# Optimization experiments

Measured on AMD Instinct MI355X. Metric: run time of the kernel, lower is better.

The kernel has to match this reference:

```python
import jax, jax.numpy as jnp
import numpy as np

EMB = 1024
HID = 4096
B = 2
T = 4096
NUM_BLOCK = 24
EPS = 1e-6


def rmsnorm(x):
    # unparameterized RMS normalization over last dim
    return x * jax.lax.rsqrt(jnp.mean(jnp.square(x), axis=-1, keepdims=True) + EPS)


def setup_inputs() -> dict:
    key = jax.random.key(0)
    k1, k2, k3, k4 = jax.random.split(key, 4)
    x = jax.random.normal(k1, (B, T, EMB), dtype=jnp.float32)
    W1 = 0.02 * jax.random.normal(k2, (HID, EMB), dtype=jnp.float32)
    W2 = 0.02 * jax.random.normal(k3, (HID, EMB), dtype=jnp.float32)
    W3 = (0.02 / np.sqrt(NUM_BLOCK)) * jax.random.normal(k4, (EMB, HID), dtype=jnp.float32)
    return {"x": x, "W1": W1, "W2": W2, "W3": W3}


def bar_quadratic_causal_preact_stable(a, b):
    # y_t = (1/t^2) * sum_{i<=t} sum_{j<=t} exp(a_i + b_j), per feature channel.
    # exp factorizes, so compute stably via log-cumsum-exp along the seq axis.
    seq = a.shape[1]
    log_t = jnp.log(jnp.arange(1, seq + 1, dtype=a.dtype))  # [T]
    la = jax.lax.cumlogsumexp(a, axis=1)  # [B,T,H]
    lb = jax.lax.cumlogsumexp(b, axis=1)  # [B,T,H]
    return jnp.exp(la + lb - 2.0 * log_t[None, :, None])


def reference(x, W1, W2, W3):
    r = rmsnorm(x)
    a = jnp.einsum('bte,he->bth', r, W1)  # fc_1, no bias
    b = jnp.einsum('bte,he->bth', r, W2)  # fc_2, no bias
    r = bar_quadratic_causal_preact_stable(a, b)
    r = rmsnorm(r)
    r = jnp.einsum('bth,eh->bte', r, W3)  # fc_3, no bias
    return x + r
```

## Files before the change

kernel.cpp:

```cpp
#include <hip/hip_runtime.h>
#include <hip/hip_fp8.h>

#define EMB 1024
#define HID 4096
#define NB 2
#define TT 4096
#define MROWS (NB*TT)
#define N1 (2*HID)
#define CHUNK 128
#define NCH 32

typedef short short8 __attribute__((ext_vector_type(8)));
typedef float v4f   __attribute__((ext_vector_type(4)));
typedef int   v4i   __attribute__((ext_vector_type(4)));
typedef int   v8i   __attribute__((ext_vector_type(8)));

__device__ __forceinline__ unsigned short f2bf(float f) {
  unsigned int u = __float_as_uint(f);
  u += 0x7FFFu + ((u >> 16) & 1u);
  return (unsigned short)(u >> 16);
}
__device__ __forceinline__ float bf2f(unsigned short s) {
  return __uint_as_float(((unsigned int)s) << 16);
}
__device__ __forceinline__ unsigned char f2e4m3(float f) {
  __hip_fp8_e4m3 q(f);
  return *(unsigned char*)&q;
}
__device__ __forceinline__ float e4m32f(unsigned char c) {
  __hip_fp8_e4m3 q = *(__hip_fp8_e4m3*)&c;
  return (float)q;
}
__device__ __forceinline__ void g2l16(const void* g, void* l) {
  __builtin_amdgcn_global_load_lds(
      (const __attribute__((address_space(1))) void*)g,
      (__attribute__((address_space(3))) void*)l, 16, 0, 0);
}

__device__ __forceinline__ float block_reduce_sum(float v, float* sbuf) {
  #pragma unroll
  for (int off = 32; off; off >>= 1) v += __shfl_down(v, off, 64);
  int lane = threadIdx.x & 63, w = threadIdx.x >> 6;
  if (lane == 0) sbuf[w] = v;
  __syncthreads();
  return sbuf[0] + sbuf[1] + sbuf[2] + sbuf[3];
}

__global__ __launch_bounds__(256) void conv_all(const float* __restrict__ W1,
                                                const float* __restrict__ W2,
                                                const float* __restrict__ W3,
                                                unsigned short* __restrict__ o12,
                                                unsigned char* __restrict__ o3) {
  size_t i = ((size_t)blockIdx.x*256 + threadIdx.x)*4;
  if (i < 2ull*HID*EMB) {
    const float* s = (i < (size_t)HID*EMB) ? (W1 + i) : (W2 + (i - (size_t)HID*EMB));
    float4 v = *(const float4*)s;
    ushort4 u; u.x=f2bf(v.x); u.y=f2bf(v.y); u.z=f2bf(v.z); u.w=f2bf(v.w);
    *(ushort4*)(o12 + i) = u;
  } else {
    size_t off = i - 2ull*HID*EMB;
    float4 v = *(const float4*)(W3 + off);
    uchar4 u; u.x=f2e4m3(v.x*64.f); u.y=f2e4m3(v.y*64.f);
             u.z=f2e4m3(v.z*64.f); u.w=f2e4m3(v.w*64.f);
    *(uchar4*)(o3 + off) = u;
  }
}

__global__ __launch_bounds__(256) void rmsnorm_x(const float* __restrict__ x,
                                                 unsigned short* __restrict__ r) {
  __shared__ float sbuf[4];
  int row = blockIdx.x;
  float4 v = *(const float4*)(x + (size_t)row*EMB + threadIdx.x*4);
  float ss = v.x*v.x + v.y*v.y + v.z*v.z + v.w*v.w;
  float tot = block_reduce_sum(ss, sbuf);
  float sc = rsqrtf(tot * (1.0f/EMB) + 1e-6f);
  ushort4 o; o.x=f2bf(v.x*sc); o.y=f2bf(v.y*sc); o.z=f2bf(v.z*sc); o.w=f2bf(v.w*sc);
  *(ushort4*)(r + (size_t)row*EMB + threadIdx.x*4) = o;
}

__global__ __launch_bounds__(256) void normq(const unsigned short* __restrict__ y,
                                             unsigned char* __restrict__ y8) {
  __shared__ float sbuf[4];
  int row = blockIdx.x;
  const unsigned short* p = y + (size_t)row*HID + threadIdx.x*16;
  short8 v0 = *(const short8*)p;
  short8 v1 = *(const short8*)(p+8);
  float f[16]; float ss = 0.f;
  #pragma unroll
  for (int j=0;j<8;++j){ f[j]=bf2f((unsigned short)v0[j]); f[j+8]=bf2f((unsigned short)v1[j]); }
  #pragma unroll
  for (int j=0;j<16;++j) ss += f[j]*f[j];
  float tot = block_reduce_sum(ss, sbuf);
  float sc = rsqrtf(tot*(1.0f/HID) + 1e-6f);
  unsigned int w[4];
  #pragma unroll
  for (int g=0; g<4; ++g) {
    unsigned int a0 = f2e4m3(f[g*4+0]*sc);
    unsigned int a1 = f2e4m3(f[g*4+1]*sc);
    unsigned int a2 = f2e4m3(f[g*4+2]*sc);
    unsigned int a3 = f2e4m3(f[g*4+3]*sc);
    w[g] = a0 | (a1<<8) | (a2<<16) | (a3<<24);
  }
  uint4 o; o.x=w[0]; o.y=w[1]; o.z=w[2]; o.w=w[3];
  *(uint4*)(y8 + (size_t)row*HID + threadIdx.x*16) = o;
}

__global__ __launch_bounds__(256, 2)
void gemm_exp(const unsigned short* __restrict__ A,
              const unsigned short* __restrict__ Bt,
              unsigned char* __restrict__ C8,
              float* __restrict__ part,
              int K, int N) {
  __shared__ short lA[128*64];
  __shared__ short lB[128*64];
  const int tid  = threadIdx.x;
  const int lane = tid & 63;
  const int wm   = (tid >> 6) >> 1, wn = (tid >> 6) & 1;
  const int bid  = blockIdx.x;
  const int s0i  = bid >> 3;
  const int rowTile = s0i >> 3;
  const int colTile = ((bid & 7) << 3) | (s0i & 7);
  const int rowBase = rowTile * 128;
  const int colBase = colTile * 128;

  v4f acc[4][4];
  #pragma unroll
  for (int i=0;i<4;++i)
    #pragma unroll
    for (int j=0;j<4;++j) acc[i][j] = (v4f){0.f,0.f,0.f,0.f};

  for (int k0 = 0; k0 < K; k0 += 64) {
    #pragma unroll
    for (int j = 0; j < 4; ++j) {
      int s = j*256 + tid;
      int m = s >> 3;
      int c = (s & 7) ^ (m & 7);
      g2l16(A + (size_t)(rowBase + m)*K + k0 + c*8, &lA[s*8]);
    }
    #pragma unroll
    for (int j = 0; j < 4; ++j) {
      int s = j*256 + tid;
      int m = s >> 3;
      int c = (s & 7) ^ (m & 7);
      g2l16(Bt + (size_t)(colBase + m)*K + k0 + c*8, &lB[s*8]);
    }
    __syncthreads();
    #pragma unroll
    for (int s2 = 0; s2 < 2; ++s2) {
      const int quad = lane >> 4;
      const int cc = s2*4 + quad;
      short8 aF[4], bF[4];
      #pragma unroll
      for (int mt = 0; mt < 4; ++mt) {
        int ml = wm*64 + mt*16 + (lane & 15);
        aF[mt] = *(const short8*)&lA[(ml*8 + (cc ^ (ml & 7)))*8];
      }
      #pragma unroll
      for (int nt = 0; nt < 4; ++nt) {
        int nl = wn*64 + nt*16 + (lane & 15);
        bF[nt] = *(const short8*)&lB[(nl*8 + (cc ^ (nl & 7)))*8];
      }
      #pragma unroll
      for (int mt = 0; mt < 4; ++mt)
        #pragma unroll
        for (int nt = 0; nt < 4; ++nt)
          acc[mt][nt] = __builtin_amdgcn_mfma_f32_16x16x32_bf16(aF[mt], bF[nt], acc[mt][nt], 0, 0, 0);
    }
    __syncthreads();
  }

  const int quad = lane >> 4, c15 = lane & 15;
  float csum[4] = {0.f, 0.f, 0.f, 0.f};
  #pragma unroll
  for (int mt = 0; mt < 4; ++mt) {
    #pragma unroll
    for (int nt = 0; nt < 4; ++nt) {
      int col = colBase + wn*64 + nt*16 + c15;
      #pragma unroll
      for (int r = 0; r < 4; ++r) {
        int row = rowBase + wm*64 + mt*16 + quad*4 + r;
        size_t idx = (size_t)row*N + col;
        float e = __expf(acc[mt][nt][r]);
        C8[idx] = f2e4m3(e);
        csum[nt] += e;
      }
    }
  }
  float* cs = (float*)lA;
  #pragma unroll
  for (int nt = 0; nt < 4; ++nt) {
    float s = csum[nt];
    s += __shfl_xor(s, 16, 64);
    s += __shfl_xor(s, 32, 64);
    if (lane < 16) cs[wm*128 + wn*64 + nt*16 + lane] = s;
  }
  __syncthreads();
  if (tid < 128)
    part[(size_t)(colBase + tid)*64 + rowTile] = cs[tid] + cs[128 + tid];
}

__global__ __launch_bounds__(256, 2)
void gemm_out(const unsigned char* __restrict__ A8,
              const unsigned char* __restrict__ B8,
              const float* __restrict__ x,
              float* __restrict__ out,
              int K, int N) {
  __shared__ unsigned char lA8[128*128];
  __shared__ unsigned char lB8[128*128];
  const int tid  = threadIdx.x;
  const int lane = tid & 63;
  const int wm   = (tid >> 6) >> 1, wn = (tid >> 6) & 1;
  const int rowBase = blockIdx.x * 128;
  const int colBase = blockIdx.y * 128;
  const int q   = lane >> 4;
  const int r15 = lane & 15;

  v4f acc[4][4];
  #pragma unroll
  for (int i=0;i<4;++i)
    #pragma unroll
    for (int j=0;j<4;++j) acc[i][j] = (v4f){0.f,0.f,0.f,0.f};

  for (int k0 = 0; k0 < K; k0 += 128) {
    #pragma unroll
    for (int j = 0; j < 4; ++j) {
      int s = j*256 + tid;
      int m = s >> 3;
      int c = (s & 7) ^ (m & 7);
      g2l16(A8 + (size_t)(rowBase + m)*K + k0 + c*16, &lA8[s*16]);
    }
    #pragma unroll
    for (int j = 0; j < 4; ++j) {
      int s = j*256 + tid;
      int m = s >> 3;
      int c = (s & 7) ^ (m & 7);
      g2l16(B8 + (size_t)(colBase + m)*K + k0 + c*16, &lB8[s*16]);
    }
    __syncthreads();
    v8i aF[4], bF[4];
    #pragma unroll
    for (int mt = 0; mt < 4; ++mt) {
      int ml = wm*64 + mt*16 + r15;
      int s  = ml & 7;
      v4i lo = *(const v4i*)&lA8[ml*128 + (((2*q)   ^ s)<<4)];
      v4i hi = *(const v4i*)&lA8[ml*128 + (((2*q+1) ^ s)<<4)];
      aF[mt] = __builtin_shufflevector(lo, hi, 0,1,2,3,4,5,6,7);
    }
    #pragma unroll
    for (int nt = 0; nt < 4; ++nt) {
      int nl = wn*64 + nt*16 + r15;
      int s  = nl & 7;
      v4i lo = *(const v4i*)&lB8[nl*128 + (((2*q)   ^ s)<<4)];
      v4i hi = *(const v4i*)&lB8[nl*128 + (((2*q+1) ^ s)<<4)];
      bF[nt] = __builtin_shufflevector(lo, hi, 0,1,2,3,4,5,6,7);
    }
    #pragma unroll
    for (int mt = 0; mt < 4; ++mt)
      #pragma unroll
      for (int nt = 0; nt < 4; ++nt)
        acc[mt][nt] = __builtin_amdgcn_mfma_scale_f32_16x16x128_f8f6f4(
            aF[mt], bF[nt], acc[mt][nt],
            0, 0,
            0, 0x7F7F7F7F,
            0, 0x7F7F7F7F);
    __syncthreads();
  }

  const int quad = lane >> 4, c15 = lane & 15;
  const float inv64 = 1.0f/64.0f;
  #pragma unroll
  for (int mt = 0; mt < 4; ++mt) {
    #pragma unroll
    for (int nt = 0; nt < 4; ++nt) {
      int col = colBase + wn*64 + nt*16 + c15;
      #pragma unroll
      for (int r = 0; r < 4; ++r) {
        int row = rowBase + wm*64 + mt*16 + quad*4 + r;
        size_t idx = (size_t)row*N + col;
        out[idx] = x[idx] + inv64*acc[mt][nt][r];
      }
    }
  }
}

__global__ __launch_bounds__(256) void scan_prefix(float* __restrict__ part) {
  int idx = blockIdx.x*256 + threadIdx.x;
  int col = idx >> 1, bb = idx & 1;
  float* p = part + (size_t)col*64 + bb*NCH;
  float run = 0.f;
  #pragma unroll
  for (int c = 0; c < NCH; ++c) { float v = p[c]; p[c] = run; run += v; }
}

__global__ __launch_bounds__(256) void scan_emit(const unsigned char* __restrict__ ab,
                                                 const float* __restrict__ part,
                                                 unsigned short* __restrict__ y) {
  int h = blockIdx.x*256 + threadIdx.x;
  int cy = blockIdx.y, bb = blockIdx.z;
  float sa = part[(size_t)h*64 + bb*NCH + cy];
  float sb = part[(size_t)(HID + h)*64 + bb*NCH + cy];
  const unsigned char* pa = ab + ((size_t)(bb*TT + cy*CHUNK))*N1 + h;
  const unsigned char* pb = pa + HID;
  unsigned short* py = y + ((size_t)(bb*TT + cy*CHUNK))*HID + h;
  int t0 = cy*CHUNK;
  #pragma unroll 4
  for (int i = 0; i < CHUNK; ++i) {
    sa += e4m32f(pa[(size_t)i*N1]);
    sb += e4m32f(pb[(size_t)i*N1]);
    float inv = 1.0f / (float)(t0 + i + 1);
    py[(size_t)i*HID] = f2bf(sa*sb*inv*inv);
  }
}

extern "C" void kernel_launch(void* const* d_in, const int* in_sizes, int n_in,
                              void* d_out, int out_size, void* d_ws, size_t ws_size,
                              hipStream_t stream) {
  const float* x  = (const float*)d_in[0];
  const float* W1 = (const float*)d_in[1];
  const float* W2 = (const float*)d_in[2];
  const float* W3 = (const float*)d_in[3];
  float* out = (float*)d_out;
  char* ws = (char*)d_ws;

  unsigned short* r_bf   = (unsigned short*)(ws);
  unsigned short* w12_bf = (unsigned short*)(ws + 16777216ull);
  unsigned char*  w3_8   = (unsigned char*) (ws + 33554432ull);
  unsigned char*  ab8    = (unsigned char*) (ws + 37748736ull);
  unsigned short* y_bf   = (unsigned short*)(ws + 104857600ull);
  unsigned char*  y8     = (unsigned char*) (ws + 171966464ull);
  float*          part   = (float*)d_out;

  conv_all<<<12288, 256, 0, stream>>>(W1, W2, W3, w12_bf, w3_8);
  rmsnorm_x<<<MROWS, 256, 0, stream>>>(x, r_bf);
  gemm_exp<<<4096, 256, 0, stream>>>(r_bf, w12_bf, ab8, part, EMB, N1);
  scan_prefix<<<64, 256, 0, stream>>>(part);
  scan_emit<<<dim3(16,NCH,2), 256, 0, stream>>>(ab8, part, y_bf);
  normq<<<MROWS, 256, 0, stream>>>(y_bf, y8);
  gemm_out<<<dim3(64,8), 256, 0, stream>>>(y8, w3_8, x, out, HID, EMB);
}
```

Baseline: 353.7 us.

## Fuse RMS norm into scan and defer row scaling to output GEMM epilogue

Removes the separate normq kernel and the bf16 intermediate y buffer. scan_emit now writes y directly as fp8 with a fixed pre-scale and accumulates per-row sums of squares via wave shuffles plus atomicAdd into a zeroed rsq buffer. gemm_out then applies the per-row rsqrt normalization in its epilogue, relying on the row scale commuting with the matmul. This saves a full write and read of the bf16 activation plus a kernel launch, at the cost of global atomics and a fixed fp8 scale that is not adapted to each row's magnitude.

```diff
diff --git a/kernel.cpp b/kernel.cpp
--- a/kernel.cpp
+++ b/kernel.cpp
@@ -78,33 +78,6 @@
   *(ushort4*)(r + (size_t)row*EMB + threadIdx.x*4) = o;
 }
 
-__global__ __launch_bounds__(256) void normq(const unsigned short* __restrict__ y,
-                                             unsigned char* __restrict__ y8) {
-  __shared__ float sbuf[4];
-  int row = blockIdx.x;
-  const unsigned short* p = y + (size_t)row*HID + threadIdx.x*16;
-  short8 v0 = *(const short8*)p;
-  short8 v1 = *(const short8*)(p+8);
-  float f[16]; float ss = 0.f;
-  #pragma unroll
-  for (int j=0;j<8;++j){ f[j]=bf2f((unsigned short)v0[j]); f[j+8]=bf2f((unsigned short)v1[j]); }
-  #pragma unroll
-  for (int j=0;j<16;++j) ss += f[j]*f[j];
-  float tot = block_reduce_sum(ss, sbuf);
-  float sc = rsqrtf(tot*(1.0f/HID) + 1e-6f);
-  unsigned int w[4];
-  #pragma unroll
-  for (int g=0; g<4; ++g) {
-    unsigned int a0 = f2e4m3(f[g*4+0]*sc);
-    unsigned int a1 = f2e4m3(f[g*4+1]*sc);
-    unsigned int a2 = f2e4m3(f[g*4+2]*sc);
-    unsigned int a3 = f2e4m3(f[g*4+3]*sc);
-    w[g] = a0 | (a1<<8) | (a2<<16) | (a3<<24);
-  }
-  uint4 o; o.x=w[0]; o.y=w[1]; o.z=w[2]; o.w=w[3];
-  *(uint4*)(y8 + (size_t)row*HID + threadIdx.x*16) = o;
-}
-
 __global__ __launch_bounds__(256, 2)
 void gemm_exp(const unsigned short* __restrict__ A,
               const unsigned short* __restrict__ Bt,
@@ -203,6 +176,7 @@
 void gemm_out(const unsigned char* __restrict__ A8,
               const unsigned char* __restrict__ B8,
               const float* __restrict__ x,
+              const float* __restrict__ rsq,
               float* __restrict__ out,
               int K, int N) {
   __shared__ unsigned char lA8[128*128];
@@ -267,7 +241,6 @@
   }
 
   const int quad = lane >> 4, c15 = lane & 15;
-  const float inv64 = 1.0f/64.0f;
   #pragma unroll
   for (int mt = 0; mt < 4; ++mt) {
     #pragma unroll
@@ -277,14 +250,17 @@
       for (int r = 0; r < 4; ++r) {
         int row = rowBase + wm*64 + mt*16 + quad*4 + r;
         size_t idx = (size_t)row*N + col;
-        out[idx] = x[idx] + inv64*acc[mt][nt][r];
+        float sc = rsqrtf(rsq[row]*(1.0f/HID) + 1e-6f) * 0.0625f;
+        out[idx] = x[idx] + sc*acc[mt][nt][r];
       }
     }
   }
 }
 
-__global__ __launch_bounds__(256) void scan_prefix(float* __restrict__ part) {
+__global__ __launch_bounds__(256) void scan_prefix(float* __restrict__ part,
+                                                   float* __restrict__ rsq) {
   int idx = blockIdx.x*256 + threadIdx.x;
+  if (idx < MROWS) rsq[idx] = 0.f;
   int col = idx >> 1, bb = idx & 1;
   float* p = part + (size_t)col*64 + bb*NCH;
   float run = 0.f;
@@ -294,21 +270,29 @@
 
 __global__ __launch_bounds__(256) void scan_emit(const unsigned char* __restrict__ ab,
                                                  const float* __restrict__ part,
-                                                 unsigned short* __restrict__ y) {
+                                                 unsigned char* __restrict__ y8,
+                                                 float* __restrict__ rsq) {
   int h = blockIdx.x*256 + threadIdx.x;
   int cy = blockIdx.y, bb = blockIdx.z;
+  int lane = threadIdx.x & 63;
   float sa = part[(size_t)h*64 + bb*NCH + cy];
   float sb = part[(size_t)(HID + h)*64 + bb*NCH + cy];
   const unsigned char* pa = ab + ((size_t)(bb*TT + cy*CHUNK))*N1 + h;
   const unsigned char* pb = pa + HID;
-  unsigned short* py = y + ((size_t)(bb*TT + cy*CHUNK))*HID + h;
+  unsigned char* py = y8 + ((size_t)(bb*TT + cy*CHUNK))*HID + h;
+  float* prs = rsq + bb*TT + cy*CHUNK;
   int t0 = cy*CHUNK;
   #pragma unroll 4
   for (int i = 0; i < CHUNK; ++i) {
     sa += e4m32f(pa[(size_t)i*N1]);
     sb += e4m32f(pb[(size_t)i*N1]);
-    float inv = 1.0f / (float)(t0 + i + 1);
-    py[(size_t)i*HID] = f2bf(sa*sb*inv*inv);
+    float inv = __builtin_amdgcn_rcpf((float)(t0 + i + 1));
+    float y = sa*sb*inv*inv;
+    py[(size_t)i*HID] = f2e4m3(y*0.25f);
+    float s2 = y*y;
+    #pragma unroll
+    for (int off = 32; off; off >>= 1) s2 += __shfl_xor(s2, off, 64);
+    if (lane == 0) atomicAdd(&prs[i], s2);
   }
 }
 
@@ -326,15 +310,14 @@
   unsigned short* w12_bf = (unsigned short*)(ws + 16777216ull);
   unsigned char*  w3_8   = (unsigned char*) (ws + 33554432ull);
   unsigned char*  ab8    = (unsigned char*) (ws + 37748736ull);
-  unsigned short* y_bf   = (unsigned short*)(ws + 104857600ull);
+  float*          rsq    = (float*)        (ws + 104857600ull);
   unsigned char*  y8     = (unsigned char*) (ws + 171966464ull);
   float*          part   = (float*)d_out;
 
   conv_all<<<12288, 256, 0, stream>>>(W1, W2, W3, w12_bf, w3_8);
   rmsnorm_x<<<MROWS, 256, 0, stream>>>(x, r_bf);
   gemm_exp<<<4096, 256, 0, stream>>>(r_bf, w12_bf, ab8, part, EMB, N1);
-  scan_prefix<<<64, 256, 0, stream>>>(part);
-  scan_emit<<<dim3(16,NCH,2), 256, 0, stream>>>(ab8, part, y_bf);
-  normq<<<MROWS, 256, 0, stream>>>(y_bf, y8);
-  gemm_out<<<dim3(64,8), 256, 0, stream>>>(y8, w3_8, x, out, HID, EMB);
-}
+  scan_prefix<<<64, 256, 0, stream>>>(part, rsq);
+  scan_emit<<<dim3(16,NCH,2), 256, 0, stream>>>(ab8, part, y8, rsq);
+  gemm_out<<<dim3(64,8), 256, 0, stream>>>(y8, w3_8, x, rsq, out, HID, EMB);
+}
```

New measurement: 406.8 us. 15.0% more time.
